# Kernel optimization log

Measured on AMD Instinct MI355X. Metric: run time of the kernel, lower is better.

## Reference

```python
import jax, jax.numpy as jnp
import numpy as np


def lstm_step(x_t, h, c, Wih, Whh, bih, bhh):
    # PyTorch LSTM gate order: i, f, g, o
    gates = x_t @ Wih.T + h @ Whh.T + bih + bhh
    i, f, g, o = jnp.split(gates, 4, axis=-1)
    i = jax.nn.sigmoid(i)
    f = jax.nn.sigmoid(f)
    g = jnp.tanh(g)
    o = jax.nn.sigmoid(o)
    c_new = f * c + i * g
    h_new = o * jnp.tanh(c_new)
    return h_new, c_new


def setup_inputs() -> dict:
    key = jax.random.key(0)
    N, C, T, V, M = 512, 3, 300, 25, 2
    F = C * V * M  # 150
    H = 100
    ks = jax.random.split(key, 12)
    s = 1.0 / np.sqrt(H)  # PyTorch LSTM/Linear init scale
    u = lambda k, shape: jax.random.uniform(k, shape, jnp.float32, -s, s)
    return {
        "x": jax.random.normal(ks[0], (N, C, T, V, M), jnp.float32),
        "enc_Wih": u(ks[1], (4 * H, F)),
        "enc_Whh": u(ks[2], (4 * H, H)),
        "enc_bih": u(ks[3], (4 * H,)),
        "enc_bhh": u(ks[4], (4 * H,)),
        "dec_Wih": u(ks[5], (4 * H, F)),
        "dec_Whh": u(ks[6], (4 * H, H)),
        "dec_bih": u(ks[7], (4 * H,)),
        "dec_bhh": u(ks[8], (4 * H,)),
        "fc_W": u(ks[9], (F, H)),
        "fc_b": u(ks[10], (F,)),
    }


def reference(x, enc_Wih, enc_Whh, enc_bih, enc_bhh,
              dec_Wih, dec_Whh, dec_bih, dec_bhh, fc_W, fc_b):
    N, C, T, V, M = x.shape
    F = C * V * M
    H = enc_Whh.shape[1]
    # (N,C,T,V,M) -> (N,T,C*V*M)
    xs = jnp.transpose(x, (0, 2, 1, 3, 4)).reshape(N, T, F)

    # Encoder LSTM: only need final (h, c)
    h0 = jnp.zeros((N, H), x.dtype)
    c0 = jnp.zeros((N, H), x.dtype)

    def enc_step(carry, xt):
        h, c = carry
        h, c = lstm_step(xt, h, c, enc_Wih, enc_Whh, enc_bih, enc_bhh)
        return (h, c), None

    (h, c), _ = jax.lax.scan(enc_step, (h0, c0), jnp.swapaxes(xs, 0, 1))

    inp0 = jnp.zeros((N, F), x.dtype)

    def dec_step(carry, _):
        inp, h, c = carry
        h, c = lstm_step(inp, h, c, dec_Wih, dec_Whh, dec_bih, dec_bhh)
        out = h @ fc_W.T + fc_b
        return (out, h, c), out

    _, outs = jax.lax.scan(dec_step, (inp0, h, c), None, length=T - 1)  # [T-1,N,F]

    # outputs[:,0,:] stays zero, like the torch.zeros buffer
    outputs = jnp.concatenate([jnp.zeros((1, N, F), x.dtype), outs], axis=0)  # [T,N,F]
    outputs = jnp.swapaxes(outputs, 0, 1).reshape(N, T, C, V, M)
    return jnp.transpose(outputs, (0, 2, 1, 3, 4))  # (N,C,T,V,M)
```

## Files before the change

kernel.cpp:

```cpp
#include <hip/hip_runtime.h>
#include <hip/hip_fp16.h>


#define B_W2P   0u
#define B_WDP   102400u
#define B_WEP   204800u
#define B_PIH   307200u
#define B_BENC  460800u
#define B_B1    462848u
#define B_BEFF  464896u
#define B_HIST  466944u
#define HIST_STRIDE 29952

typedef _Float16 h2_t __attribute__((ext_vector_type(2)));
typedef _Float16 f16x8 __attribute__((ext_vector_type(8)));
typedef float f32x4v __attribute__((ext_vector_type(4)));

#if defined(__has_builtin)
#if __has_builtin(__builtin_amdgcn_fdot2)
#define HAS_FDOT2 1
#endif
#endif

__device__ __forceinline__ float fdot2u(unsigned a, unsigned b, float c) {
#ifdef HAS_FDOT2
  return __builtin_amdgcn_fdot2(__builtin_bit_cast(h2_t, a), __builtin_bit_cast(h2_t, b), c, false);
#else
  float al = __half2float(__ushort_as_half((unsigned short)(a & 0xffffu)));
  float ah = __half2float(__ushort_as_half((unsigned short)(a >> 16)));
  float bl = __half2float(__ushort_as_half((unsigned short)(b & 0xffffu)));
  float bh = __half2float(__ushort_as_half((unsigned short)(b >> 16)));
  return fmaf(ah, bh, fmaf(al, bl, c));
#endif
}

__device__ __forceinline__ unsigned pack2f(float a, float b) {
  return (unsigned)__half_as_ushort(__float2half(a)) |
         ((unsigned)__half_as_ushort(__float2half(b)) << 16);
}

__device__ __forceinline__ float fast_sig(float x) {
  float e = __builtin_amdgcn_exp2f(x * -1.442695040888963f);
  return __builtin_amdgcn_rcpf(1.f + e);
}
__device__ __forceinline__ float fast_tanh(float x) {
  float e = __builtin_amdgcn_exp2f(x * -2.885390081777926f);
  return fmaf(2.f, __builtin_amdgcn_rcpf(1.f + e), -1.f);
}

__device__ __forceinline__ f32x4v mfma16(uint4 a, uint4 b, f32x4v c) {
  return __builtin_amdgcn_mfma_f32_16x16x32_f16(
      __builtin_bit_cast(f16x8, a), __builtin_bit_cast(f16x8, b), c, 0, 0, 0);
}

__device__ __forceinline__ void block_sync_lds() {
  __builtin_amdgcn_sched_barrier(0);
  asm volatile("s_waitcnt lgkmcnt(0)" ::: "memory");
  __builtin_amdgcn_s_barrier();
  __builtin_amdgcn_sched_barrier(0);
}

__global__ void prep(const float* __restrict__ dWih, const float* __restrict__ dWhh,
                     const float* __restrict__ dbih, const float* __restrict__ dbhh,
                     const float* __restrict__ eWih, const float* __restrict__ eWhh,
                     const float* __restrict__ ebih, const float* __restrict__ ebhh,
                     const float* __restrict__ fcW,  const float* __restrict__ fcb,
                     char* __restrict__ wsb)
{
  int idx = blockIdx.x * 256 + threadIdx.x;
  if (idx < 25600) {
    int q = idx >> 9, t = idx & 511;
    unsigned w2p = 0, wdp = 0, wep = 0;
    if (t < 400) {
      int r = (t & 3) * 100 + (t >> 2);
      int j0 = 2 * q, j1 = 2 * q + 1;
      float wd0 = dWhh[r * 100 + j0], wd1 = dWhh[r * 100 + j1];
      float we0 = eWhh[r * 100 + j0], we1 = eWhh[r * 100 + j1];
      float s0 = 0.f, s1 = 0.f;
      for (int f = 0; f < 150; ++f) {
        float a = dWih[r * 150 + f];
        s0 = fmaf(a, fcW[f * 100 + j0], s0);
        s1 = fmaf(a, fcW[f * 100 + j1], s1);
      }
      w2p = pack2f(wd0 + s0, wd1 + s1);
      wdp = pack2f(wd0, wd1);
      wep = pack2f(we0, we1);
    }
    ((unsigned*)(wsb + B_W2P))[idx] = w2p;
    ((unsigned*)(wsb + B_WDP))[idx] = wdp;
    ((unsigned*)(wsb + B_WEP))[idx] = wep;
  } else if (idx < 25600 + 38400) {
    int k = idx - 25600; int d = k >> 9, t = k & 511;
    unsigned pk = 0;
    if (t < 400) {
      int r = (t & 3) * 100 + (t >> 2);
      pk = pack2f(eWih[r * 150 + 2 * d], eWih[r * 150 + 2 * d + 1]);
    }
    ((unsigned*)(wsb + B_PIH))[k] = pk;
  } else if (idx < 25600 + 38400 + 512) {
    int t = idx - (25600 + 38400);
    float be = 0.f, b1 = 0.f, bf = 0.f;
    if (t < 400) {
      int r = (t & 3) * 100 + (t >> 2);
      be = ebih[r] + ebhh[r];
      b1 = dbih[r] + dbhh[r];
      float acc = 0.f;
      for (int f = 0; f < 150; ++f) acc = fmaf(dWih[r * 150 + f], fcb[f], acc);
      bf = b1 + acc;
    }
    ((float*)(wsb + B_BENC))[t] = be;
    ((float*)(wsb + B_B1))[t]   = b1;
    ((float*)(wsb + B_BEFF))[t] = bf;
  }
}

__global__ __launch_bounds__(512)
void recurrent(const float* __restrict__ x, char* __restrict__ wsb)
{
  const int tid  = threadIdx.x;
  const int w    = tid >> 6;
  const int lane = tid & 63;
  const int sp   = lane & 15;
  const int q    = lane >> 4;
  const int nb   = blockIdx.x * 16;

  __shared__ unsigned short hx[2][16][264];
  for (int k = tid; k < 2 * 16 * 264; k += 512) ((unsigned short*)hx)[k] = 0;

  const unsigned* WEP = (const unsigned*)(wsb + B_WEP);
  const unsigned* WDP = (const unsigned*)(wsb + B_WDP);
  const unsigned* W2P = (const unsigned*)(wsb + B_W2P);
  const unsigned* PIH = (const unsigned*)(wsb + B_PIH);

  const int nt = (w == 0) ? 4 : 3;
  int cells[4];
  float4 bs[4];
  uint4 af[4][8];
#pragma unroll
  for (int i = 0; i < 4; ++i) {
    const int tile = (i < nt) ? (w + 8 * i) : 0;
    const int col = tile * 16 + sp;
    cells[i] = 4 * tile + q;
#pragma unroll
    for (int kk = 0; kk < 8; ++kk) {
      unsigned e[4];
#pragma unroll
      for (int l = 0; l < 4; ++l) {
        const int p = kk * 16 + q * 4 + l;
        unsigned v = 0u;
        if (p < 50) v = WEP[p * 512 + col];
        else if (p < 125) v = PIH[(p - 50) * 512 + col];
        e[l] = v;
      }
      af[i][kk] = make_uint4(e[0], e[1], e[2], e[3]);
    }
    bs[i] = ((const float4*)(wsb + B_BENC))[cells[i]];
  }

  const bool stg = tid < 400;
  const int ssp = tid / 25;
  const int sr  = tid - ssp * 25;
  const float* xb = x + (size_t)(nb + (stg ? ssp : 0)) * 45000;
  int soff[6];
#pragma unroll
  for (int l = 0; l < 6; ++l) {
    const int f = sr * 6 + l;
    const int cd = f / 50;
    soff[l] = cd * 15000 + (f - cd * 50);
  }
  const int sdst = (stg ? ssp : 0) * 264 + 100 + sr * 6;

  unsigned short* histn = (unsigned short*)(wsb + B_HIST) + (size_t)(nb + sp) * HIST_STRIDE;

  __syncthreads();
  float xW[6];
  if (stg) {
    float x0[6];
#pragma unroll
    for (int l = 0; l < 6; ++l) x0[l] = xb[soff[l]];
    unsigned short* d = &hx[0][0][0] + sdst;
    *(unsigned*)(d + 0) = pack2f(x0[0], x0[1]);
    *(unsigned*)(d + 2) = pack2f(x0[2], x0[3]);
    *(unsigned*)(d + 4) = pack2f(x0[4], x0[5]);
#pragma unroll
    for (int l = 0; l < 6; ++l) xW[l] = xb[soff[l] + 50];
  }
  __syncthreads();

  float cst[4] = {0.f, 0.f, 0.f, 0.f};

  for (int t = 0; t < 300; ++t) {
    const int rd = t & 1, wr = rd ^ 1;
    if (stg && t < 299) {
      unsigned short* d = &hx[wr][0][0] + sdst;
      *(unsigned*)(d + 0) = pack2f(xW[0], xW[1]);
      *(unsigned*)(d + 2) = pack2f(xW[2], xW[3]);
      *(unsigned*)(d + 4) = pack2f(xW[4], xW[5]);
    }
    float xL[6];
    if (stg && t < 298) {
      const int to = (t + 2) * 50;
#pragma unroll
      for (int l = 0; l < 6; ++l) xL[l] = xb[soff[l] + to];
    }
    f32x4v acc[4];
#pragma unroll
    for (int i = 0; i < 4; ++i) {
      acc[i][0] = bs[i].x; acc[i][1] = bs[i].y;
      acc[i][2] = bs[i].z; acc[i][3] = bs[i].w;
    }
#pragma unroll
    for (int kk = 0; kk < 8; ++kk) {
      uint4 b = *(const uint4*)(&hx[rd][sp][kk * 32 + q * 8]);
#pragma unroll
      for (int i = 0; i < 4; ++i)
        if (i < nt) acc[i] = mfma16(af[i][kk], b, acc[i]);
    }
#pragma unroll
    for (int i = 0; i < 4; ++i) {
      if (i < nt) {
        float ii = fast_sig(acc[i][0]), ff = fast_sig(acc[i][1]);
        float gg = fast_tanh(acc[i][2]), oo = fast_sig(acc[i][3]);
        cst[i] = fmaf(ff, cst[i], ii * gg);
        float h = oo * fast_tanh(cst[i]);
        hx[wr][sp][cells[i]] = __half_as_ushort(__float2half(h));
      }
    }
    block_sync_lds();
    if (stg) {
#pragma unroll
      for (int l = 0; l < 6; ++l) xW[l] = xL[l];
    }
  }

  auto loadA4 = [&](const unsigned* W, unsigned bofs) {
#pragma unroll
    for (int i = 0; i < 4; ++i) {
      const int tile = (i < nt) ? (w + 8 * i) : 0;
      const int col = tile * 16 + sp;
#pragma unroll
      for (int kk = 0; kk < 4; ++kk) {
        unsigned e[4];
#pragma unroll
        for (int l = 0; l < 4; ++l) {
          const int p = kk * 16 + q * 4 + l;
          e[l] = (p < 50) ? W[p * 512 + col] : 0u;
        }
        af[i][kk] = make_uint4(e[0], e[1], e[2], e[3]);
      }
      bs[i] = ((const float4*)(wsb + bofs))[cells[i]];
    }
  };

  loadA4(WDP, B_B1);
  {
    f32x4v acc[4];
#pragma unroll
    for (int i = 0; i < 4; ++i) {
      acc[i][0] = bs[i].x; acc[i][1] = bs[i].y;
      acc[i][2] = bs[i].z; acc[i][3] = bs[i].w;
    }
#pragma unroll
    for (int kk = 0; kk < 4; ++kk) {
      uint4 b = *(const uint4*)(&hx[0][sp][kk * 32 + q * 8]);
#pragma unroll
      for (int i = 0; i < 4; ++i)
        if (i < nt) acc[i] = mfma16(af[i][kk], b, acc[i]);
    }
#pragma unroll
    for (int i = 0; i < 4; ++i) {
      if (i < nt) {
        float ii = fast_sig(acc[i][0]), ff = fast_sig(acc[i][1]);
        float gg = fast_tanh(acc[i][2]), oo = fast_sig(acc[i][3]);
        cst[i] = fmaf(ff, cst[i], ii * gg);
        float h = oo * fast_tanh(cst[i]);
        hx[1][sp][cells[i]] = __half_as_ushort(__float2half(h));
        histn[cells[i]] = __half_as_ushort(__float2half(h));
      }
    }
    block_sync_lds();
  }
  loadA4(W2P, B_BEFF);
  for (int s = 2; s <= 299; ++s) {
    const int rd = (299 + s) & 1, wr = rd ^ 1;
    f32x4v acc[4];
#pragma unroll
    for (int i = 0; i < 4; ++i) {
      acc[i][0] = bs[i].x; acc[i][1] = bs[i].y;
      acc[i][2] = bs[i].z; acc[i][3] = bs[i].w;
    }
#pragma unroll
    for (int kk = 0; kk < 4; ++kk) {
      uint4 b = *(const uint4*)(&hx[rd][sp][kk * 32 + q * 8]);
#pragma unroll
      for (int i = 0; i < 4; ++i)
        if (i < nt) acc[i] = mfma16(af[i][kk], b, acc[i]);
    }
#pragma unroll
    for (int i = 0; i < 4; ++i) {
      if (i < nt) {
        float ii = fast_sig(acc[i][0]), ff = fast_sig(acc[i][1]);
        float gg = fast_tanh(acc[i][2]), oo = fast_sig(acc[i][3]);
        cst[i] = fmaf(ff, cst[i], ii * gg);
        float h = oo * fast_tanh(cst[i]);
        hx[wr][sp][cells[i]] = __half_as_ushort(__float2half(h));
        histn[(s - 1) * 100 + cells[i]] = __half_as_ushort(__float2half(h));
      }
    }
    block_sync_lds();
  }
}

__global__ __launch_bounds__(192, 4)
void emit(const char* __restrict__ wsb, const float* __restrict__ fcW,
          const float* __restrict__ fcb, float* __restrict__ out)
{
  const int f = threadIdx.x;
  const int n = blockIdx.x;
  const int z = blockIdx.y;
  __shared__ unsigned short hl[15008];

  const uint4* src = (const uint4*)((const unsigned short*)(wsb + B_HIST) +
                                    (size_t)n * HIST_STRIDE + z * 15000);
  for (int k = f; k < 1875; k += 192) ((uint4*)hl)[k] = src[k];

  const bool on = f < 150;
  unsigned fw[50];
  float bias = 0.f;
  if (on) {
    const float* fp = fcW + f * 100;
#pragma unroll
    for (int q = 0; q < 50; ++q) fw[q] = pack2f(fp[2 * q], fp[2 * q + 1]);
    bias = fcb[f];
  }
  __syncthreads();

  if (!on) return;
  const int cc = f / 50, r = f - cc * 50;
  float* ob = out + (size_t)n * 45000 + cc * 15000 + r;
  if (z == 0) ob[0] = 0.f;
  const int rows = z ? 149 : 150;
  for (int tl = 0; tl < rows; ++tl) {
    const uint4* row = (const uint4*)(hl + tl * 100);
    float a0 = bias, a1 = 0.f, a2 = 0.f, a3 = 0.f;
#pragma unroll
    for (int ch = 0; ch < 12; ++ch) {
      uint4 v = row[ch];
      a0 = fdot2u(fw[4 * ch + 0], v.x, a0);
      a1 = fdot2u(fw[4 * ch + 1], v.y, a1);
      a2 = fdot2u(fw[4 * ch + 2], v.z, a2);
      a3 = fdot2u(fw[4 * ch + 3], v.w, a3);
    }
    uint2 v2 = *(const uint2*)(hl + tl * 100 + 96);
    a0 = fdot2u(fw[48], v2.x, a0);
    a1 = fdot2u(fw[49], v2.y, a1);
    const int tt = z * 150 + tl + 1;
    ob[tt * 50] = (a0 + a1) + (a2 + a3);
  }
}

extern "C" void kernel_launch(void* const* d_in, const int* in_sizes, int n_in,
                              void* d_out, int out_size, void* d_ws, size_t ws_size,
                              hipStream_t stream) {
  const float* x    = (const float*)d_in[0];
  const float* eWih = (const float*)d_in[1];
  const float* eWhh = (const float*)d_in[2];
  const float* ebih = (const float*)d_in[3];
  const float* ebhh = (const float*)d_in[4];
  const float* dWih = (const float*)d_in[5];
  const float* dWhh = (const float*)d_in[6];
  const float* dbih = (const float*)d_in[7];
  const float* dbhh = (const float*)d_in[8];
  const float* fcW  = (const float*)d_in[9];
  const float* fcb  = (const float*)d_in[10];
  float* out = (float*)d_out;
  char* wsb  = (char*)d_ws;

  prep<<<252, 256, 0, stream>>>(dWih, dWhh, dbih, dbhh, eWih, eWhh, ebih, ebhh, fcW, fcb, wsb);
  recurrent<<<32, 512, 0, stream>>>(x, wsb);
  emit<<<dim3(512, 2), 192, 0, stream>>>(wsb, fcW, fcb, out);
}
```

Baseline: 1.217 ms.

## Process two 16-sequence groups per recurrent block to interleave independent MFMA chains

Each recurrent block now handles 32 sequences as two independent groups that share the register-resident weight fragments. Their MFMA chains and gate activations are interleaved, so the per-step latency of one group can overlap with the other. The grid shrinks from 32 to 16 blocks and LDS for the hidden/input buffers doubles. The cost is fewer active CUs, more registers for a second accumulator set, and a longer serial critical path per step.

```diff
diff --git a/kernel.cpp b/kernel.cpp
--- a/kernel.cpp
+++ b/kernel.cpp
@@ -122,10 +122,10 @@
   const int lane = tid & 63;
   const int sp   = lane & 15;
   const int q    = lane >> 4;
-  const int nb   = blockIdx.x * 16;
-
-  __shared__ unsigned short hx[2][16][264];
-  for (int k = tid; k < 2 * 16 * 264; k += 512) ((unsigned short*)hx)[k] = 0;
+  const int nb   = blockIdx.x * 32;
+
+  __shared__ unsigned short hx[2][2][16][264];
+  for (int k = tid; k < 2 * 2 * 16 * 264; k += 512) ((unsigned short*)hx)[k] = 0;
 
   const unsigned* WEP = (const unsigned*)(wsb + B_WEP);
   const unsigned* WDP = (const unsigned*)(wsb + B_WDP);
@@ -160,7 +160,8 @@
   const bool stg = tid < 400;
   const int ssp = tid / 25;
   const int sr  = tid - ssp * 25;
-  const float* xb = x + (size_t)(nb + (stg ? ssp : 0)) * 45000;
+  const float* xbA = x + (size_t)(nb + (stg ? ssp : 0)) * 45000;
+  const float* xbB = x + (size_t)(nb + 16 + (stg ? ssp : 0)) * 45000;
   int soff[6];
 #pragma unroll
   for (int l = 0; l < 6; ++l) {
@@ -170,66 +171,83 @@
   }
   const int sdst = (stg ? ssp : 0) * 264 + 100 + sr * 6;
 
-  unsigned short* histn = (unsigned short*)(wsb + B_HIST) + (size_t)(nb + sp) * HIST_STRIDE;
+  unsigned short* histA = (unsigned short*)(wsb + B_HIST) + (size_t)(nb + sp) * HIST_STRIDE;
+  unsigned short* histB = (unsigned short*)(wsb + B_HIST) + (size_t)(nb + 16 + sp) * HIST_STRIDE;
 
   __syncthreads();
-  float xW[6];
+  float xWA[6], xWB[6];
   if (stg) {
-    float x0[6];
-#pragma unroll
-    for (int l = 0; l < 6; ++l) x0[l] = xb[soff[l]];
-    unsigned short* d = &hx[0][0][0] + sdst;
-    *(unsigned*)(d + 0) = pack2f(x0[0], x0[1]);
-    *(unsigned*)(d + 2) = pack2f(x0[2], x0[3]);
-    *(unsigned*)(d + 4) = pack2f(x0[4], x0[5]);
-#pragma unroll
-    for (int l = 0; l < 6; ++l) xW[l] = xb[soff[l] + 50];
+    float a0[6], b0[6];
+#pragma unroll
+    for (int l = 0; l < 6; ++l) { a0[l] = xbA[soff[l]]; b0[l] = xbB[soff[l]]; }
+    unsigned short* dA = &hx[0][0][0][0] + sdst;
+    unsigned short* dB = &hx[1][0][0][0] + sdst;
+    *(unsigned*)(dA + 0) = pack2f(a0[0], a0[1]);
+    *(unsigned*)(dA + 2) = pack2f(a0[2], a0[3]);
+    *(unsigned*)(dA + 4) = pack2f(a0[4], a0[5]);
+    *(unsigned*)(dB + 0) = pack2f(b0[0], b0[1]);
+    *(unsigned*)(dB + 2) = pack2f(b0[2], b0[3]);
+    *(unsigned*)(dB + 4) = pack2f(b0[4], b0[5]);
+#pragma unroll
+    for (int l = 0; l < 6; ++l) { xWA[l] = xbA[soff[l] + 50]; xWB[l] = xbB[soff[l] + 50]; }
   }
   __syncthreads();
 
-  float cst[4] = {0.f, 0.f, 0.f, 0.f};
+  float cst[2][4] = {{0.f, 0.f, 0.f, 0.f}, {0.f, 0.f, 0.f, 0.f}};
 
   for (int t = 0; t < 300; ++t) {
     const int rd = t & 1, wr = rd ^ 1;
     if (stg && t < 299) {
-      unsigned short* d = &hx[wr][0][0] + sdst;
-      *(unsigned*)(d + 0) = pack2f(xW[0], xW[1]);
-      *(unsigned*)(d + 2) = pack2f(xW[2], xW[3]);
-      *(unsigned*)(d + 4) = pack2f(xW[4], xW[5]);
-    }
-    float xL[6];
+      unsigned short* dA = &hx[0][wr][0][0] + sdst;
+      unsigned short* dB = &hx[1][wr][0][0] + sdst;
+      *(unsigned*)(dA + 0) = pack2f(xWA[0], xWA[1]);
+      *(unsigned*)(dA + 2) = pack2f(xWA[2], xWA[3]);
+      *(unsigned*)(dA + 4) = pack2f(xWA[4], xWA[5]);
+      *(unsigned*)(dB + 0) = pack2f(xWB[0], xWB[1]);
+      *(unsigned*)(dB + 2) = pack2f(xWB[2], xWB[3]);
+      *(unsigned*)(dB + 4) = pack2f(xWB[4], xWB[5]);
+    }
+    float xLA[6], xLB[6];
     if (stg && t < 298) {
       const int to = (t + 2) * 50;
 #pragma unroll
-      for (int l = 0; l < 6; ++l) xL[l] = xb[soff[l] + to];
-    }
-    f32x4v acc[4];
-#pragma unroll
-    for (int i = 0; i < 4; ++i) {
-      acc[i][0] = bs[i].x; acc[i][1] = bs[i].y;
-      acc[i][2] = bs[i].z; acc[i][3] = bs[i].w;
-    }
+      for (int l = 0; l < 6; ++l) { xLA[l] = xbA[soff[l] + to]; xLB[l] = xbB[soff[l] + to]; }
+    }
+    f32x4v acc[2][4];
+#pragma unroll
+    for (int g = 0; g < 2; ++g)
+#pragma unroll
+      for (int i = 0; i < 4; ++i) {
+        acc[g][i][0] = bs[i].x; acc[g][i][1] = bs[i].y;
+        acc[g][i][2] = bs[i].z; acc[g][i][3] = bs[i].w;
+      }
 #pragma unroll
     for (int kk = 0; kk < 8; ++kk) {
-      uint4 b = *(const uint4*)(&hx[rd][sp][kk * 32 + q * 8]);
+      uint4 bA = *(const uint4*)(&hx[0][rd][sp][kk * 32 + q * 8]);
+      uint4 bB = *(const uint4*)(&hx[1][rd][sp][kk * 32 + q * 8]);
 #pragma unroll
       for (int i = 0; i < 4; ++i)
-        if (i < nt) acc[i] = mfma16(af[i][kk], b, acc[i]);
-    }
-#pragma unroll
-    for (int i = 0; i < 4; ++i) {
-      if (i < nt) {
-        float ii = fast_sig(acc[i][0]), ff = fast_sig(acc[i][1]);
-        float gg = fast_tanh(acc[i][2]), oo = fast_sig(acc[i][3]);
-        cst[i] = fmaf(ff, cst[i], ii * gg);
-        float h = oo * fast_tanh(cst[i]);
-        hx[wr][sp][cells[i]] = __half_as_ushort(__float2half(h));
-      }
-    }
+        if (i < nt) {
+          acc[0][i] = mfma16(af[i][kk], bA, acc[0][i]);
+          acc[1][i] = mfma16(af[i][kk], bB, acc[1][i]);
+        }
+    }
+#pragma unroll
+    for (int g = 0; g < 2; ++g)
+#pragma unroll
+      for (int i = 0; i < 4; ++i) {
+        if (i < nt) {
+          float ii = fast_sig(acc[g][i][0]), ff = fast_sig(acc[g][i][1]);
+          float gg = fast_tanh(acc[g][i][2]), oo = fast_sig(acc[g][i][3]);
+          cst[g][i] = fmaf(ff, cst[g][i], ii * gg);
+          float h = oo * fast_tanh(cst[g][i]);
+          hx[g][wr][sp][cells[i]] = __half_as_ushort(__float2half(h));
+        }
+      }
     block_sync_lds();
     if (stg) {
 #pragma unroll
-      for (int l = 0; l < 6; ++l) xW[l] = xL[l];
+      for (int l = 0; l < 6; ++l) { xWA[l] = xLA[l]; xWB[l] = xLB[l]; }
     }
   }
 
@@ -254,59 +272,75 @@
 
   loadA4(WDP, B_B1);
   {
-    f32x4v acc[4];
-#pragma unroll
-    for (int i = 0; i < 4; ++i) {
-      acc[i][0] = bs[i].x; acc[i][1] = bs[i].y;
-      acc[i][2] = bs[i].z; acc[i][3] = bs[i].w;
-    }
+    f32x4v acc[2][4];
+#pragma unroll
+    for (int g = 0; g < 2; ++g)
+#pragma unroll
+      for (int i = 0; i < 4; ++i) {
+        acc[g][i][0] = bs[i].x; acc[g][i][1] = bs[i].y;
+        acc[g][i][2] = bs[i].z; acc[g][i][3] = bs[i].w;
+      }
 #pragma unroll
     for (int kk = 0; kk < 4; ++kk) {
-      uint4 b = *(const uint4*)(&hx[0][sp][kk * 32 + q * 8]);
+      uint4 bA = *(const uint4*)(&hx[0][0][sp][kk * 32 + q * 8]);
+      uint4 bB = *(const uint4*)(&hx[1][0][sp][kk * 32 + q * 8]);
 #pragma unroll
       for (int i = 0; i < 4; ++i)
-        if (i < nt) acc[i] = mfma16(af[i][kk], b, acc[i]);
-    }
-#pragma unroll
-    for (int i = 0; i < 4; ++i) {
-      if (i < nt) {
-        float ii = fast_sig(acc[i][0]), ff = fast_sig(acc[i][1]);
-        float gg = fast_tanh(acc[i][2]), oo = fast_sig(acc[i][3]);
-        cst[i] = fmaf(ff, cst[i], ii * gg);
-        float h = oo * fast_tanh(cst[i]);
-        hx[1][sp][cells[i]] = __half_as_ushort(__float2half(h));
-        histn[cells[i]] = __half_as_ushort(__float2half(h));
-      }
-    }
+        if (i < nt) {
+          acc[0][i] = mfma16(af[i][kk], bA, acc[0][i]);
+          acc[1][i] = mfma16(af[i][kk], bB, acc[1][i]);
+        }
+    }
+#pragma unroll
+    for (int g = 0; g < 2; ++g)
+#pragma unroll
+      for (int i = 0; i < 4; ++i) {
+        if (i < nt) {
+          float ii = fast_sig(acc[g][i][0]), ff = fast_sig(acc[g][i][1]);
+          float gg = fast_tanh(acc[g][i][2]), oo = fast_sig(acc[g][i][3]);
+          cst[g][i] = fmaf(ff, cst[g][i], ii * gg);
+          float h = oo * fast_tanh(cst[g][i]);
+          hx[g][1][sp][cells[i]] = __half_as_ushort(__float2half(h));
+          (g ? histB : histA)[cells[i]] = __half_as_ushort(__float2half(h));
+        }
+      }
     block_sync_lds();
   }
   loadA4(W2P, B_BEFF);
   for (int s = 2; s <= 299; ++s) {
     const int rd = (299 + s) & 1, wr = rd ^ 1;
-    f32x4v acc[4];
-#pragma unroll
-    for (int i = 0; i < 4; ++i) {
-      acc[i][0] = bs[i].x; acc[i][1] = bs[i].y;
-      acc[i][2] = bs[i].z; acc[i][3] = bs[i].w;
-    }
+    f32x4v acc[2][4];
+#pragma unroll
+    for (int g = 0; g < 2; ++g)
+#pragma unroll
+      for (int i = 0; i < 4; ++i) {
+        acc[g][i][0] = bs[i].x; acc[g][i][1] = bs[i].y;
+        acc[g][i][2] = bs[i].z; acc[g][i][3] = bs[i].w;
+      }
 #pragma unroll
     for (int kk = 0; kk < 4; ++kk) {
-      uint4 b = *(const uint4*)(&hx[rd][sp][kk * 32 + q * 8]);
+      uint4 bA = *(const uint4*)(&hx[0][rd][sp][kk * 32 + q * 8]);
+      uint4 bB = *(const uint4*)(&hx[1][rd][sp][kk * 32 + q * 8]);
 #pragma unroll
       for (int i = 0; i < 4; ++i)
-        if (i < nt) acc[i] = mfma16(af[i][kk], b, acc[i]);
-    }
-#pragma unroll
-    for (int i = 0; i < 4; ++i) {
-      if (i < nt) {
-        float ii = fast_sig(acc[i][0]), ff = fast_sig(acc[i][1]);
-        float gg = fast_tanh(acc[i][2]), oo = fast_sig(acc[i][3]);
-        cst[i] = fmaf(ff, cst[i], ii * gg);
-        float h = oo * fast_tanh(cst[i]);
-        hx[wr][sp][cells[i]] = __half_as_ushort(__float2half(h));
-        histn[(s - 1) * 100 + cells[i]] = __half_as_ushort(__float2half(h));
-      }
-    }
+        if (i < nt) {
+          acc[0][i] = mfma16(af[i][kk], bA, acc[0][i]);
+          acc[1][i] = mfma16(af[i][kk], bB, acc[1][i]);
+        }
+    }
+#pragma unroll
+    for (int g = 0; g < 2; ++g)
+#pragma unroll
+      for (int i = 0; i < 4; ++i) {
+        if (i < nt) {
+          float ii = fast_sig(acc[g][i][0]), ff = fast_sig(acc[g][i][1]);
+          float gg = fast_tanh(acc[g][i][2]), oo = fast_sig(acc[g][i][3]);
+          cst[g][i] = fmaf(ff, cst[g][i], ii * gg);
+          float h = oo * fast_tanh(cst[g][i]);
+          hx[g][wr][sp][cells[i]] = __half_as_ushort(__float2half(h));
+          (g ? histB : histA)[(s - 1) * 100 + cells[i]] = __half_as_ushort(__float2half(h));
+        }
+      }
     block_sync_lds();
   }
 }
@@ -377,6 +411,6 @@
   char* wsb  = (char*)d_ws;
 
   prep<<<252, 256, 0, stream>>>(dWih, dWhh, dbih, dbhh, eWih, eWhh, ebih, ebhh, fcW, fcb, wsb);
-  recurrent<<<32, 512, 0, stream>>>(x, wsb);
+  recurrent<<<16, 512, 0, stream>>>(x, wsb);
   emit<<<dim3(512, 2), 192, 0, stream>>>(wsb, fcW, fcb, out);
 }
```

Measured after the change: 1.882 ms. 1.55x slower.
